# Optimization experiments

Measured on AMD Instinct MI355X. Metric: run time of the kernel, lower is better.

Reference implementation:

```python
import jax, jax.numpy as jnp
import numpy as np

B, N, M, C, K = 4, 4096, 4096, 64, 32
RADIUS = 0.1
EPS = 1e-5


def setup_inputs() -> dict:
    key = jax.random.key(0)
    ks = jax.random.split(key, 32)
    inp = {
        "query_xyz": jax.random.uniform(ks[0], (B, N, 3), jnp.float32),
        "support_xyz": jax.random.uniform(ks[1], (B, M, 3), jnp.float32),
        "query_mask": jax.random.randint(ks[2], (B, N), 0, 2, jnp.int32),
        "support_mask": jax.random.randint(ks[3], (B, M), 0, 2, jnp.int32),
        "support_features": jax.random.normal(ks[4], (B, C, M), jnp.float32),
    }
    names = ["theta1", "theta2", "phi", "psi", "alpha", "gamma1", "gamma2"]
    in_ch = {"theta1": 3}
    for j, nm in enumerate(names):
        inp[f"W_{nm}"] = jax.random.normal(ks[5 + j], (C, in_ch.get(nm, C)), jnp.float32) * 0.05
        inp[f"b_{nm}"] = jax.random.normal(ks[12 + j], (C,), jnp.float32) * 0.05
    for j, nm in enumerate(["theta", "gamma"]):
        inp[f"g_{nm}"] = 1.0 + 0.1 * jax.random.normal(ks[19 + 2 * j], (C,), jnp.float32)
        inp[f"be_{nm}"] = 0.1 * jax.random.normal(ks[20 + 2 * j], (C,), jnp.float32)
        inp[f"rm_{nm}"] = jnp.zeros((C,), jnp.float32)
        inp[f"rv_{nm}"] = jnp.ones((C,), jnp.float32)
    return inp


def _conv(W, b, x):
    # 1x1 Conv2d: channelwise linear on [B, C_in, N, K]
    return jnp.einsum('oc,bcnk->bonk', W, x) + b[None, :, None, None]


def _bn(x, g, be, rm, rv):
    # BatchNorm2d, inference form with running stats
    inv = g / jnp.sqrt(rv + EPS)
    return x * inv[None, :, None, None] + (be - rm * inv)[None, :, None, None]


def _forward(query_xyz, support_xyz, query_mask, support_mask, support_features, P):
    Bq, Nq = query_xyz.shape[:2]
    # pairwise squared distances [B, N, M]; masked support pushed to +inf
    d2 = jnp.sum((query_xyz[:, :, None, :] - support_xyz[:, None, :, :]) ** 2, axis=-1)
    d2 = jnp.where(support_mask[:, None, :] > 0, d2, jnp.inf)
    # ball query as K-nearest-within-radius
    neg, idx = jax.lax.top_k(-d2, K)                    # idx: [B, N, K]
    nbr_mask = (-neg) <= RADIUS ** 2                    # valid-neighbor mask
    flat = idx.reshape(Bq, Nq * K)
    x_j = jnp.take_along_axis(support_features, flat[:, None, :], axis=2).reshape(Bq, -1, Nq, K)
    g_xyz = jnp.take_along_axis(support_xyz, flat[:, :, None], axis=1).reshape(Bq, Nq, K, 3)
    # normalize_xyz=True -> offsets divided by radius; layout [B, 3, N, K]
    pos = ((g_xyz - query_xyz[:, :, None, :]) / RADIUS).transpose(0, 3, 1, 2)
    # nearest-neighbor query for x_i [B, C, N]
    idx_nn = jnp.argmin(d2, axis=-1)
    x_i = jnp.take_along_axis(support_features, idx_nn[:, None, :], axis=2)
    # positional encoding delta
    delta = jax.nn.relu(_bn(_conv(P['W_theta2'], P['b_theta2'],
                                  _conv(P['W_theta1'], P['b_theta1'], pos)),
                            P['g_theta'], P['be_theta'], P['rm_theta'], P['rv_theta']))
    lin_i = _conv(P['W_phi'], P['b_phi'], x_i[..., None])   # [B,C,N,1], broadcast over K
    lin_j = _conv(P['W_psi'], P['b_psi'], x_j)
    rel = lin_i - lin_j + delta
    rel = jax.nn.relu(_bn(_conv(P['W_gamma2'], P['b_gamma2'],
                                _conv(P['W_gamma1'], P['b_gamma1'], rel)),
                          P['g_gamma'], P['be_gamma'], P['rm_gamma'], P['rv_gamma']))
    weights = jax.nn.softmax(rel, axis=-1)                   # softmax over neighbor axis
    feats = _conv(P['W_alpha'], P['b_alpha'], x_j) + delta
    fmask = nbr_mask.astype(feats.dtype) + (1.0 - query_mask.astype(feats.dtype))[:, :, None]
    feats = feats * fmask[:, None, :, :]
    return jnp.sum(weights * feats, axis=-1)                 # [B, C, N]


def reference(query_xyz, support_xyz, query_mask, support_mask, support_features,
              W_theta1, b_theta1, W_theta2, b_theta2, W_phi, b_phi, W_psi, b_psi,
              W_alpha, b_alpha, W_gamma1, b_gamma1, W_gamma2, b_gamma2,
              g_theta, be_theta, rm_theta, rv_theta, g_gamma, be_gamma, rm_gamma, rv_gamma):
    P = dict(locals())
    return _forward(query_xyz, support_xyz, query_mask, support_mask, support_features, P)
```

## Files before the change

kernel.cpp:

```cpp
#include <hip/hip_runtime.h>
#include <cstdint>
#include <cstddef>

#define NN 4096
#define MM 4096
#define CC 64
#define KK 32
#define INF_F __builtin_huge_valf()

#define SC 2304
#define CCAP 2560

typedef __bf16 bf16x8 __attribute__((ext_vector_type(8)));
typedef __bf16 bf16x4 __attribute__((ext_vector_type(4)));
typedef float f32x16 __attribute__((ext_vector_type(16)));

#define NFRAG 40
#define ASTRIDE 68
#define ESTRIDE 36

#define WFENCE() asm volatile("s_waitcnt lgkmcnt(0)" ::: "memory")

__device__ __forceinline__ f32x16 zero16() {
  f32x16 z;
#pragma unroll
  for (int i = 0; i < 16; ++i) z[i] = 0.0f;
  return z;
}

__device__ __forceinline__ void conv1(const bf16x8* Wr, int conv,
                                      const bf16x8* B4, f32x16& a0, f32x16& a1) {
#pragma unroll
  for (int s = 0; s < 4; ++s) {
    a0 = __builtin_amdgcn_mfma_f32_32x32x16_bf16(Wr[(conv * 2 + 0) * 4 + s], B4[s], a0, 0, 0, 0);
    a1 = __builtin_amdgcn_mfma_f32_32x32x16_bf16(Wr[(conv * 2 + 1) * 4 + s], B4[s], a1, 0, 0, 0);
  }
}

__device__ __forceinline__ void sort64(float& v, int& i, int lane) {
#pragma unroll
  for (int k = 2; k <= 64; k <<= 1) {
#pragma unroll
    for (int j = k >> 1; j > 0; j >>= 1) {
      const float ov = __shfl_xor(v, j);
      const int oi = __shfl_xor(i, j);
      const bool up = ((lane & k) == 0);
      const bool lower = ((lane & j) == 0);
      const bool take = (up == lower) ? (ov < v) : (ov > v);
      if (take) { v = ov; i = oi; }
    }
  }
}

__device__ __forceinline__ void insert_cands(float vv, int ii, float& sv, int& si,
                                             float& cmax, int lane) {
  unsigned long long cand = __ballot(vv < cmax);
  while (cand) {
    const int src = __ffsll((unsigned long long)cand) - 1;
    cand &= cand - 1;
    const float dc = __shfl(vv, src);
    if (dc < cmax) {
      const int im = __shfl(ii, src);
      const float up_s = __shfl_up(sv, 1);
      const int up_i = __shfl_up(si, 1);
      const bool pg = sv > dc;
      const bool pgu = (lane > 0) && (up_s > dc);
      const float ns = pg ? (pgu ? up_s : dc) : sv;
      const int ni = pg ? (pgu ? up_i : im) : si;
      if (lane < 32) { sv = ns; si = ni; }
      cmax = __shfl(sv, 31);
    }
  }
}

__global__ void pt_prep(const float* __restrict__ sf, const float* __restrict__ sxyz,
                        __bf16* __restrict__ ftb, float4* __restrict__ sx4) {
  const int b = blockIdx.x >> 4;
  const int m = ((blockIdx.x & 15) << 8) + threadIdx.x;
  float v[CC];
#pragma unroll
  for (int c = 0; c < CC; ++c) v[c] = sf[((size_t)(b * CC + c)) * MM + m];
  bf16x8* db = (bf16x8*)(ftb + ((size_t)(b * MM + m)) * CC);
#pragma unroll
  for (int i = 0; i < CC / 8; ++i) {
    bf16x8 t;
#pragma unroll
    for (int j = 0; j < 8; ++j) t[j] = (__bf16)v[8 * i + j];
    db[i] = t;
  }
  const size_t g = (size_t)(b * MM + m);
  sx4[g] = make_float4(sxyz[g * 3 + 0], sxyz[g * 3 + 1], sxyz[g * 3 + 2], 0.0f);
}

__global__ void pt_compact(const float* __restrict__ sxyz, const int* __restrict__ smask,
                           float4* __restrict__ cpts) {
  __shared__ int lcount;
  const int b = blockIdx.x;
  const int tid = threadIdx.x;
  const int lane = tid & 63;
  if (tid == 0) lcount = 0;
  __syncthreads();
  float4* dst = cpts + (size_t)b * CCAP;
#pragma unroll
  for (int r = 0; r < 4; ++r) {
    const int m = r * 1024 + tid;
    const size_t g = (size_t)b * MM + m;
    const bool valid = smask[g] > 0;
    float x = 0, y = 0, z = 0;
    if (valid) { x = sxyz[g * 3 + 0]; y = sxyz[g * 3 + 1]; z = sxyz[g * 3 + 2]; }
    const unsigned long long mask = __ballot(valid);
    const int pre = (int)__popcll(mask & ((1ull << lane) - 1ull));
    int wbase = 0;
    if (lane == 0) wbase = atomicAdd(&lcount, (int)__popcll(mask));
    wbase = __shfl(wbase, 0);
    if (valid) dst[wbase + pre] = make_float4(x, y, z, __int_as_float(m));
  }
  __syncthreads();
  const int cnt = lcount;
  for (int i = cnt + tid; i < SC; i += 1024)
    dst[i] = make_float4(1e4f, 1e4f, 1e4f, __int_as_float(0));
}

__global__ void pt_pack(const float* __restrict__ Wpsi, const float* __restrict__ W2,
                        const float* __restrict__ Wg1, const float* __restrict__ Wg2,
                        const float* __restrict__ Wa, __bf16* __restrict__ Wpack) {
  const int t = blockIdx.x * 256 + threadIdx.x;
  if (t >= NFRAG * 64) return;
  const int lane = t & 63;
  const int fi = t >> 6;
  const int s = fi & 3;
  const int mt = (fi >> 2) & 1;
  const int conv = fi >> 3;
  const float* W = conv == 0 ? Wpsi : conv == 1 ? W2 : conv == 2 ? Wg1 : conv == 3 ? Wg2 : Wa;
  const int m = mt * 32 + (lane & 31);
  const int k0 = s * 16 + (lane >> 5) * 8;
  bf16x8 vh;
#pragma unroll
  for (int j = 0; j < 8; ++j) vh[j] = (__bf16)W[m * CC + k0 + j];
  ((bf16x8*)Wpack)[fi * 64 + lane] = vh;
}

__global__ void pt_packphi(const float* __restrict__ Wphi, float* __restrict__ WphiT) {
  const int t = blockIdx.x * 256 + threadIdx.x;
  if (t >= CC * CC) return;
  const int c = t >> 6, o = t & 63;
  WphiT[t] = Wphi[o * CC + c];
}

__global__ void pt_packc(const float* __restrict__ gT, const float* __restrict__ beT,
                         const float* __restrict__ rmT, const float* __restrict__ rvT,
                         const float* __restrict__ gG, const float* __restrict__ beG,
                         const float* __restrict__ rmG, const float* __restrict__ rvG,
                         const float* __restrict__ b2, const float* __restrict__ bg1,
                         const float* __restrict__ bg2, const float* __restrict__ ba,
                         float4* __restrict__ eo, float4* __restrict__ bo) {
  const int o = threadIdx.x;
  if (o >= CC) return;
  const float invT = gT[o] / sqrtf(rvT[o] + 1e-5f);
  const float invG = gG[o] / sqrtf(rvG[o] + 1e-5f);
  eo[o] = make_float4(invT, beT[o] - rmT[o] * invT, invG, beG[o] - rmG[o] * invG);
  bo[o] = make_float4(b2[o], bg1[o], bg2[o], ba[o]);
}

__global__ void pt_knn(const float* __restrict__ qxyz, const float4* __restrict__ cpts,
                       const __bf16* __restrict__ ftb,
                       const float* __restrict__ WphiT, const float* __restrict__ bphi,
                       const float* __restrict__ bpsi,
                       int* __restrict__ oidx, unsigned* __restrict__ ovalid,
                       float* __restrict__ lin) {
  const int lane = threadIdx.x & 63;
  const int qi = blockIdx.x * 4 + (threadIdx.x >> 6);
  const int b = qi >> 12;
  const float qx = qxyz[qi * 3 + 0];
  const float qy = qxyz[qi * 3 + 1];
  const float qz = qxyz[qi * 3 + 2];
  const float4* sb = cpts + (size_t)b * CCAP;

  float v0 = INF_F, v1 = INF_F, v2 = INF_F, v3 = INF_F;
  int i0 = 0, i1 = 0, i2 = 0, i3 = 0;
#pragma unroll 1
  for (int j = 0; j < 36; j += 4) {
    float4 P[4];
#pragma unroll
    for (int u = 0; u < 4; ++u) P[u] = sb[(j + u) * 64 + lane];
#pragma unroll
    for (int u = 0; u < 4; ++u) {
      const float dx = P[u].x - qx, dy = P[u].y - qy, dz = P[u].z - qz;
      const float d = dx * dx + dy * dy + dz * dz;
      const int m = __float_as_int(P[u].w);
      const bool c3 = d < v3, c2 = d < v2, c1 = d < v1, c0 = d < v0;
      v3 = c3 ? (c2 ? v2 : d) : v3;  i3 = c3 ? (c2 ? i2 : m) : i3;
      v2 = c2 ? (c1 ? v1 : d) : v2;  i2 = c2 ? (c1 ? i1 : m) : i2;
      v1 = c1 ? (c0 ? v0 : d) : v1;  i1 = c1 ? (c0 ? i0 : m) : i1;
      v0 = c0 ? d : v0;              i0 = c0 ? m : i0;
    }
  }

  float sv = v0;
  int si = i0;
  sort64(sv, si, lane);
  float cmax = __shfl(sv, 31);
  insert_cands(v1, i1, sv, si, cmax, lane);
  insert_cands(v2, i2, sv, si, cmax, lane);
  insert_cands(v3, i3, sv, si, cmax, lane);

  if (__ballot(v3 < cmax)) {
    {
      const float4 p = sb[lane];
      const float dx = p.x - qx, dy = p.y - qy, dz = p.z - qz;
      float v = dx * dx + dy * dy + dz * dz;
      int id = __float_as_int(p.w);
      sort64(v, id, lane);
      sv = v; si = id;
    }
    cmax = __shfl(sv, 31);
    for (int m0 = 64; m0 < SC; m0 += 64) {
      const float4 p = sb[m0 + lane];
      const float dx = p.x - qx, dy = p.y - qy, dz = p.z - qz;
      const float d = dx * dx + dy * dy + dz * dz;
      insert_cands(d, __float_as_int(p.w), sv, si, cmax, lane);
    }
  }

  if (lane < 32) oidx[(size_t)qi * KK + lane] = si;
  const unsigned long long vb = __ballot((lane < 32) && (sv <= 0.01f));
  if (lane == 0) ovalid[qi] = (unsigned)(vb & 0xffffffffull);

  const int nnb = __shfl(si, 0);
  const bf16x8* xr = (const bf16x8*)(ftb + ((size_t)(b * MM + nnb)) * CC);
  float a = bphi[lane] - bpsi[lane];
#pragma unroll
  for (int i = 0; i < 8; ++i) {
    const bf16x8 xv = xr[i];
#pragma unroll
    for (int j = 0; j < 8; ++j) a += WphiT[(8 * i + j) * CC + lane] * (float)xv[j];
  }
  lin[qi * CC + lane] = a;
}

__launch_bounds__(256, 2)
__global__ void pt_fused(
    const float* __restrict__ qxyz, const float4* __restrict__ sx4,
    const int* __restrict__ qmask, const __bf16* __restrict__ ftb,
    const int* __restrict__ kidx, const unsigned* __restrict__ kvalid,
    const float* __restrict__ lin,
    const float* __restrict__ W1, const float* __restrict__ b1,
    const __bf16* __restrict__ Wpack, const float4* __restrict__ eo,
    const float4* __restrict__ bo, float* __restrict__ out) {
  __shared__ float EPI[4][CC * ESTRIDE];
  __shared__ float4 sEO[CC], sBO[CC];
  const int wid = threadIdx.x >> 6;
  const int lane = threadIdx.x & 63;
  const int g = lane >> 5;
  const int col = lane & 31;
  const int q = blockIdx.x * 4 + wid;
  const int b = q >> 12;
  const int nq = q & (NN - 1);
  float* epi = EPI[wid];
  __bf16* act = (__bf16*)epi;
  const bf16x8* Wf = (const bf16x8*)Wpack;

  bf16x8 Wr[NFRAG];
#pragma unroll
  for (int f = 0; f < NFRAG; ++f) Wr[f] = Wf[f * 64 + lane];

  sEO[lane] = eo[lane];
  sBO[lane] = bo[lane];

  const int idx = kidx[q * KK + col];
  const float fm = (float)((kvalid[q] >> col) & 1u) + 1.0f - (float)qmask[q];

  bf16x8 Xb[4];
  {
    const __bf16* ftq = ftb + ((size_t)(b * MM + idx)) * CC;
#pragma unroll
    for (int s = 0; s < 4; ++s) Xb[s] = *(const bf16x8*)(ftq + s * 16 + g * 8);
  }

  bf16x8 Tb[4];
  {
    const float qx = qxyz[q * 3 + 0], qy = qxyz[q * 3 + 1], qz = qxyz[q * 3 + 2];
    const float4 pj = sx4[(size_t)b * MM + idx];
    const float p0 = (pj.x - qx) * 10.0f;
    const float p1 = (pj.y - qy) * 10.0f;
    const float p2 = (pj.z - qz) * 10.0f;
#pragma unroll
    for (int s = 0; s < 4; ++s) {
      bf16x8 t;
#pragma unroll
      for (int j = 0; j < 8; ++j) {
        const int c = s * 16 + g * 8 + j;
        t[j] = (__bf16)(b1[c] + W1[c * 3 + 0] * p0 + W1[c * 3 + 1] * p1 + W1[c * 3 + 2] * p2);
      }
      Tb[s] = t;
    }
  }
  WFENCE();

  float DELv[32];
  {
    f32x16 aT0 = zero16(), aT1 = zero16(), aP0 = zero16(), aP1 = zero16();
    conv1(Wr, 1, Tb, aT0, aT1);
    conv1(Wr, 0, Xb, aP0, aP1);
#pragma unroll
    for (int mt = 0; mt < 2; ++mt)
#pragma unroll
      for (int t = 0; t < 4; ++t) {
        const int ob = mt * 32 + 8 * t + 4 * g;
        const float4 lv = *(const float4*)(lin + q * CC + ob);
        const float lva[4] = {lv.x, lv.y, lv.z, lv.w};
        bf16x4 w;
#pragma unroll
        for (int i = 0; i < 4; ++i) {
          const int r = t * 4 + i;
          const int o = ob + i;
          const float4 e = sEO[o];
          const float dv = fmaxf(((mt ? aT1[r] : aT0[r]) + sBO[o].x) * e.x + e.y, 0.0f);
          DELv[mt * 16 + r] = dv;
          w[i] = (__bf16)(lva[i] - (mt ? aP1[r] : aP0[r]) + dv);
        }
        *(bf16x4*)(act + col * ASTRIDE + ob) = w;
      }
  }
  WFENCE();

  f32x16 fa0 = zero16(), fa1 = zero16();
  {
    bf16x8 Rb[4];
#pragma unroll
    for (int s = 0; s < 4; ++s) {
      const bf16x4 lo = *(const bf16x4*)(act + col * ASTRIDE + s * 16 + g * 8);
      const bf16x4 hi = *(const bf16x4*)(act + col * ASTRIDE + s * 16 + g * 8 + 4);
      Rb[s] = bf16x8{lo[0], lo[1], lo[2], lo[3], hi[0], hi[1], hi[2], hi[3]};
    }
    f32x16 a0 = zero16(), a1 = zero16();
    conv1(Wr, 2, Rb, a0, a1);
    conv1(Wr, 4, Xb, fa0, fa1);
#pragma unroll
    for (int mt = 0; mt < 2; ++mt)
#pragma unroll
      for (int t = 0; t < 4; ++t) {
        const int ob = mt * 32 + 8 * t + 4 * g;
        bf16x4 w;
#pragma unroll
        for (int i = 0; i < 4; ++i) {
          const int r = t * 4 + i;
          w[i] = (__bf16)((mt ? a1[r] : a0[r]) + sBO[ob + i].y);
        }
        *(bf16x4*)(act + col * ASTRIDE + ob) = w;
      }
  }
  WFENCE();

  f32x16 h0 = zero16(), h1 = zero16();
  {
    bf16x8 Rb[4];
#pragma unroll
    for (int s = 0; s < 4; ++s) {
      const bf16x4 lo = *(const bf16x4*)(act + col * ASTRIDE + s * 16 + g * 8);
      const bf16x4 hi = *(const bf16x4*)(act + col * ASTRIDE + s * 16 + g * 8 + 4);
      Rb[s] = bf16x8{lo[0], lo[1], lo[2], lo[3], hi[0], hi[1], hi[2], hi[3]};
    }
    conv1(Wr, 3, Rb, h0, h1);
  }
  WFENCE();

#pragma unroll
  for (int mt = 0; mt < 2; ++mt)
#pragma unroll
    for (int t = 0; t < 4; ++t)
#pragma unroll
      for (int i = 0; i < 4; ++i) {
        const int r = t * 4 + i;
        const int o = mt * 32 + 4 * g + 8 * t + i;
        const float4 e = sEO[o];
        const float v = fmaxf(((mt ? h1[r] : h0[r]) + sBO[o].z) * e.z + e.w, 0.0f);
        epi[o * ESTRIDE + col] = v;
      }
  WFENCE();

  float ev[32];
  float sum;
  {
    const float* row = epi + lane * ESTRIDE;
    float mx = -INF_F;
#pragma unroll
    for (int n = 0; n < 32; n += 4) {
      const float4 t = *(const float4*)(row + n);
      ev[n] = t.x; ev[n + 1] = t.y; ev[n + 2] = t.z; ev[n + 3] = t.w;
      mx = fmaxf(mx, fmaxf(fmaxf(t.x, t.y), fmaxf(t.z, t.w)));
    }
    sum = 0.0f;
#pragma unroll
    for (int n = 0; n < 32; ++n) { ev[n] = __expf(ev[n] - mx); sum += ev[n]; }
  }
  WFENCE();

#pragma unroll
  for (int mt = 0; mt < 2; ++mt)
#pragma unroll
    for (int t = 0; t < 4; ++t)
#pragma unroll
      for (int i = 0; i < 4; ++i) {
        const int r = t * 4 + i;
        const int o = mt * 32 + 4 * g + 8 * t + i;
        const float f = ((mt ? fa1[r] : fa0[r]) + sBO[o].w + DELv[mt * 16 + r]) * fm;
        epi[o * ESTRIDE + col] = f;
      }
  WFENCE();

  {
    const float* row = epi + lane * ESTRIDE;
    float acc = 0.0f;
#pragma unroll
    for (int n = 0; n < 32; n += 4) {
      const float4 t = *(const float4*)(row + n);
      acc += ev[n] * t.x + ev[n + 1] * t.y + ev[n + 2] * t.z + ev[n + 3] * t.w;
    }
    out[((size_t)(b * CC + lane)) * NN + nq] = acc * __builtin_amdgcn_rcpf(sum);
  }
}

extern "C" void kernel_launch(void* const* d_in, const int* in_sizes, int n_in,
                              void* d_out, int out_size, void* d_ws, size_t ws_size,
                              hipStream_t stream) {
  (void)in_sizes; (void)n_in; (void)out_size; (void)ws_size;
  const float* qxyz = (const float*)d_in[0];
  const float* sxyz = (const float*)d_in[1];
  const int* qmask = (const int*)d_in[2];
  const int* smask = (const int*)d_in[3];
  const float* sfeat = (const float*)d_in[4];
  const float* W1 = (const float*)d_in[5];
  const float* b1 = (const float*)d_in[6];
  const float* W2 = (const float*)d_in[7];
  const float* b2 = (const float*)d_in[8];
  const float* Wphi = (const float*)d_in[9];
  const float* bphi = (const float*)d_in[10];
  const float* Wpsi = (const float*)d_in[11];
  const float* bpsi = (const float*)d_in[12];
  const float* Wa = (const float*)d_in[13];
  const float* ba = (const float*)d_in[14];
  const float* Wg1 = (const float*)d_in[15];
  const float* bg1 = (const float*)d_in[16];
  const float* Wg2 = (const float*)d_in[17];
  const float* bg2 = (const float*)d_in[18];
  const float* gT = (const float*)d_in[19];
  const float* beT = (const float*)d_in[20];
  const float* rmT = (const float*)d_in[21];
  const float* rvT = (const float*)d_in[22];
  const float* gG = (const float*)d_in[23];
  const float* beG = (const float*)d_in[24];
  const float* rmG = (const float*)d_in[25];
  const float* rvG = (const float*)d_in[26];

  char* ws = (char*)d_ws;
  int* kidx      = (int*)(ws + 0);
  unsigned* kval = (unsigned*)(ws + 2097152);
  __bf16* ftb    = (__bf16*)(ws + 2162688);
  float4* sx4    = (float4*)(ws + 4259840);
  float* lin     = (float*)(ws + 4521984);
  __bf16* Wpack  = (__bf16*)(ws + 8716288);
  float4* eo     = (float4*)(ws + 8757248);
  float4* bo     = (float4*)(ws + 8758272);
  float4* cpts   = (float4*)(ws + 8759296);
  float* WphiT   = (float*)(ws + 8923136);

  hipLaunchKernelGGL(pt_prep, dim3(64), dim3(256), 0, stream, sfeat, sxyz, ftb, sx4);
  hipLaunchKernelGGL(pt_compact, dim3(4), dim3(1024), 0, stream, sxyz, smask, cpts);
  hipLaunchKernelGGL(pt_pack, dim3(10), dim3(256), 0, stream, Wpsi, W2, Wg1, Wg2, Wa, Wpack);
  hipLaunchKernelGGL(pt_packphi, dim3(16), dim3(256), 0, stream, Wphi, WphiT);
  hipLaunchKernelGGL(pt_packc, dim3(1), dim3(64), 0, stream,
                     gT, beT, rmT, rvT, gG, beG, rmG, rvG, b2, bg1, bg2, ba, eo, bo);
  hipLaunchKernelGGL(pt_knn, dim3(4096), dim3(256), 0, stream,
                     qxyz, cpts, ftb, WphiT, bphi, bpsi, kidx, kval, lin);
  hipLaunchKernelGGL(pt_fused, dim3(4096), dim3(256), 0, stream,
                     qxyz, sx4, qmask, ftb, kidx, kval, lin,
                     W1, b1, Wpack, eo, bo, (float*)d_out);
}
```

Before: 261.7 us.

## Merge weight-pack kernels, raise fused occupancy, shorten accumulator live ranges

Three small weight and constant packing kernels are folded into one launch to cut launch overhead. In the fused kernel, the launch-bounds minimum blocks per SM goes from 2 to 3. The theta and psi conv accumulators are split into separate scopes, and the alpha conv is deferred until after the softmax, so fewer MFMA accumulators are live at once. The aim is to lower register pressure so the tighter bound fits without spilling; the risk is spills or less instruction overlap.

```diff
diff --git a/kernel.cpp b/kernel.cpp
--- a/kernel.cpp
+++ b/kernel.cpp
@@ -121,45 +121,45 @@
     dst[i] = make_float4(1e4f, 1e4f, 1e4f, __int_as_float(0));
 }
 
-__global__ void pt_pack(const float* __restrict__ Wpsi, const float* __restrict__ W2,
-                        const float* __restrict__ Wg1, const float* __restrict__ Wg2,
-                        const float* __restrict__ Wa, __bf16* __restrict__ Wpack) {
+__global__ void pt_packall(const float* __restrict__ Wpsi, const float* __restrict__ W2,
+                           const float* __restrict__ Wg1, const float* __restrict__ Wg2,
+                           const float* __restrict__ Wa, const float* __restrict__ Wphi,
+                           const float* __restrict__ gT, const float* __restrict__ beT,
+                           const float* __restrict__ rmT, const float* __restrict__ rvT,
+                           const float* __restrict__ gG, const float* __restrict__ beG,
+                           const float* __restrict__ rmG, const float* __restrict__ rvG,
+                           const float* __restrict__ b2, const float* __restrict__ bg1,
+                           const float* __restrict__ bg2, const float* __restrict__ ba,
+                           __bf16* __restrict__ Wpack, float* __restrict__ WphiT,
+                           float4* __restrict__ eo, float4* __restrict__ bo) {
   const int t = blockIdx.x * 256 + threadIdx.x;
-  if (t >= NFRAG * 64) return;
-  const int lane = t & 63;
-  const int fi = t >> 6;
-  const int s = fi & 3;
-  const int mt = (fi >> 2) & 1;
-  const int conv = fi >> 3;
-  const float* W = conv == 0 ? Wpsi : conv == 1 ? W2 : conv == 2 ? Wg1 : conv == 3 ? Wg2 : Wa;
-  const int m = mt * 32 + (lane & 31);
-  const int k0 = s * 16 + (lane >> 5) * 8;
-  bf16x8 vh;
-#pragma unroll
-  for (int j = 0; j < 8; ++j) vh[j] = (__bf16)W[m * CC + k0 + j];
-  ((bf16x8*)Wpack)[fi * 64 + lane] = vh;
-}
-
-__global__ void pt_packphi(const float* __restrict__ Wphi, float* __restrict__ WphiT) {
-  const int t = blockIdx.x * 256 + threadIdx.x;
-  if (t >= CC * CC) return;
-  const int c = t >> 6, o = t & 63;
-  WphiT[t] = Wphi[o * CC + c];
-}
-
-__global__ void pt_packc(const float* __restrict__ gT, const float* __restrict__ beT,
-                         const float* __restrict__ rmT, const float* __restrict__ rvT,
-                         const float* __restrict__ gG, const float* __restrict__ beG,
-                         const float* __restrict__ rmG, const float* __restrict__ rvG,
-                         const float* __restrict__ b2, const float* __restrict__ bg1,
-                         const float* __restrict__ bg2, const float* __restrict__ ba,
-                         float4* __restrict__ eo, float4* __restrict__ bo) {
-  const int o = threadIdx.x;
-  if (o >= CC) return;
-  const float invT = gT[o] / sqrtf(rvT[o] + 1e-5f);
-  const float invG = gG[o] / sqrtf(rvG[o] + 1e-5f);
-  eo[o] = make_float4(invT, beT[o] - rmT[o] * invT, invG, beG[o] - rmG[o] * invG);
-  bo[o] = make_float4(b2[o], bg1[o], bg2[o], ba[o]);
+  if (t < NFRAG * 64) {
+    const int lane = t & 63;
+    const int fi = t >> 6;
+    const int s = fi & 3;
+    const int mt = (fi >> 2) & 1;
+    const int conv = fi >> 3;
+    const float* W = conv == 0 ? Wpsi : conv == 1 ? W2 : conv == 2 ? Wg1 : conv == 3 ? Wg2 : Wa;
+    const int m = mt * 32 + (lane & 31);
+    const int k0 = s * 16 + (lane >> 5) * 8;
+    bf16x8 vh;
+#pragma unroll
+    for (int j = 0; j < 8; ++j) vh[j] = (__bf16)W[m * CC + k0 + j];
+    ((bf16x8*)Wpack)[fi * 64 + lane] = vh;
+    return;
+  }
+  const int t2 = t - NFRAG * 64;
+  if (t2 < CC * CC) {
+    WphiT[t2] = Wphi[(t2 & 63) * CC + (t2 >> 6)];
+    return;
+  }
+  const int o = t2 - CC * CC;
+  if (o < CC) {
+    const float invT = gT[o] / sqrtf(rvT[o] + 1e-5f);
+    const float invG = gG[o] / sqrtf(rvG[o] + 1e-5f);
+    eo[o] = make_float4(invT, beT[o] - rmT[o] * invT, invG, beG[o] - rmG[o] * invG);
+    bo[o] = make_float4(b2[o], bg1[o], bg2[o], ba[o]);
+  }
 }
 
 __global__ void pt_knn(const float* __restrict__ qxyz, const float4* __restrict__ cpts,
@@ -238,7 +238,7 @@
   lin[qi * CC + lane] = a;
 }
 
-__launch_bounds__(256, 2)
+__launch_bounds__(256, 3)
 __global__ void pt_fused(
     const float* __restrict__ qxyz, const float4* __restrict__ sx4,
     const int* __restrict__ qmask, const __bf16* __restrict__ ftb,
@@ -299,8 +299,23 @@
 
   float DELv[32];
   {
-    f32x16 aT0 = zero16(), aT1 = zero16(), aP0 = zero16(), aP1 = zero16();
+    f32x16 aT0 = zero16(), aT1 = zero16();
     conv1(Wr, 1, Tb, aT0, aT1);
+#pragma unroll
+    for (int mt = 0; mt < 2; ++mt)
+#pragma unroll
+      for (int t = 0; t < 4; ++t)
+#pragma unroll
+        for (int i = 0; i < 4; ++i) {
+          const int r = t * 4 + i;
+          const int o = mt * 32 + 8 * t + 4 * g + i;
+          const float4 e = sEO[o];
+          DELv[mt * 16 + r] = fmaxf(((mt ? aT1[r] : aT0[r]) + sBO[o].x) * e.x + e.y, 0.0f);
+        }
+  }
+
+  {
+    f32x16 aP0 = zero16(), aP1 = zero16();
     conv1(Wr, 0, Xb, aP0, aP1);
 #pragma unroll
     for (int mt = 0; mt < 2; ++mt)
@@ -313,18 +328,13 @@
 #pragma unroll
         for (int i = 0; i < 4; ++i) {
           const int r = t * 4 + i;
-          const int o = ob + i;
-          const float4 e = sEO[o];
-          const float dv = fmaxf(((mt ? aT1[r] : aT0[r]) + sBO[o].x) * e.x + e.y, 0.0f);
-          DELv[mt * 16 + r] = dv;
-          w[i] = (__bf16)(lva[i] - (mt ? aP1[r] : aP0[r]) + dv);
+          w[i] = (__bf16)(lva[i] - (mt ? aP1[r] : aP0[r]) + DELv[mt * 16 + r]);
         }
         *(bf16x4*)(act + col * ASTRIDE + ob) = w;
       }
   }
   WFENCE();
 
-  f32x16 fa0 = zero16(), fa1 = zero16();
   {
     bf16x8 Rb[4];
 #pragma unroll
@@ -335,7 +345,6 @@
     }
     f32x16 a0 = zero16(), a1 = zero16();
     conv1(Wr, 2, Rb, a0, a1);
-    conv1(Wr, 4, Xb, fa0, fa1);
 #pragma unroll
     for (int mt = 0; mt < 2; ++mt)
 #pragma unroll
@@ -395,6 +404,9 @@
     for (int n = 0; n < 32; ++n) { ev[n] = __expf(ev[n] - mx); sum += ev[n]; }
   }
   WFENCE();
+
+  f32x16 fa0 = zero16(), fa1 = zero16();
+  conv1(Wr, 4, Xb, fa0, fa1);
 
 #pragma unroll
   for (int mt = 0; mt < 2; ++mt)
@@ -467,10 +479,10 @@
 
   hipLaunchKernelGGL(pt_prep, dim3(64), dim3(256), 0, stream, sfeat, sxyz, ftb, sx4);
   hipLaunchKernelGGL(pt_compact, dim3(4), dim3(1024), 0, stream, sxyz, smask, cpts);
-  hipLaunchKernelGGL(pt_pack, dim3(10), dim3(256), 0, stream, Wpsi, W2, Wg1, Wg2, Wa, Wpack);
-  hipLaunchKernelGGL(pt_packphi, dim3(16), dim3(256), 0, stream, Wphi, WphiT);
-  hipLaunchKernelGGL(pt_packc, dim3(1), dim3(64), 0, stream,
-                     gT, beT, rmT, rvT, gG, beG, rmG, rvG, b2, bg1, bg2, ba, eo, bo);
+  hipLaunchKernelGGL(pt_packall, dim3(27), dim3(256), 0, stream,
+                     Wpsi, W2, Wg1, Wg2, Wa, Wphi,
+                     gT, beT, rmT, rvT, gG, beG, rmG, rvG, b2, bg1, bg2, ba,
+                     Wpack, WphiT, eo, bo);
   hipLaunchKernelGGL(pt_knn, dim3(4096), dim3(256), 0, stream,
                      qxyz, cpts, ftb, WphiT, bphi, bpsi, kidx, kval, lin);
   hipLaunchKernelGGL(pt_fused, dim3(4096), dim3(256), 0, stream,
```

New measurement: 332.5 us. +27.0%, slower.
